# Kernel tuning notes

Hardware: AMD Instinct MI355X
Metric: run time of the kernel (lower is better)

The kernel has to match this reference:

```python
import jax, jax.numpy as jnp
import numpy as np

B, T = 4096, 256
COND, INTV, H = 128, 64, 256


def _glorot(key, shape):
    fan_in = shape[0]
    return jax.random.normal(key, shape, dtype=jnp.float32) / np.sqrt(fan_in)


def setup_inputs() -> dict:
    key = jax.random.key(0)
    ks = jax.random.split(key, 20)
    inp = {
        "cond": jax.random.normal(ks[0], (B, COND), dtype=jnp.float32),
        "interval_feat": jax.random.normal(ks[1], (B, INTV), dtype=jnp.float32),
        "times": jnp.cumsum(jax.random.uniform(ks[2], (B, T), dtype=jnp.float32), axis=1),
        "seq_lens": jax.random.randint(ks[3], (B,), 1, T + 1),
        # seq_feature MLP: INTV -> 2*INTV -> 2*INTV -> INTV
        "w1": _glorot(ks[4], (INTV, 2 * INTV)), "b1": jnp.zeros((2 * INTV,), jnp.float32),
        "w2": _glorot(ks[5], (2 * INTV, 2 * INTV)), "b2": jnp.zeros((2 * INTV,), jnp.float32),
        "w3": _glorot(ks[6], (2 * INTV, INTV)), "b3": jnp.zeros((INTV,), jnp.float32),
        # h0 projection: (COND+INTV) -> H
        "w_h0": _glorot(ks[7], (COND + INTV, H)), "b_h0": jnp.zeros((H,), jnp.float32),
        # GRUCell (input dim 1), gate order r,z,n
        "w_ih": _glorot(ks[8], (1, 3 * H)), "b_ih": jnp.zeros((3 * H,), jnp.float32),
        "w_hh": _glorot(ks[9], (H, 3 * H)), "b_hh": jnp.zeros((3 * H,), jnp.float32),
        # head: H -> 2 (delta, stop logit)
        "w_head": _glorot(ks[10], (H, 2)), "b_head": jnp.zeros((2,), jnp.float32),
    }
    return inp


def reference(cond, interval_feat, times, seq_lens,
              w1, b1, w2, b2, w3, b3, w_h0, b_h0,
              w_ih, w_hh, b_ih, b_hh, w_head, b_head):
    # seq_feature MLP
    s = jax.nn.relu(interval_feat @ w1 + b1)
    s = jax.nn.relu(s @ w2 + b2)
    seq_emb = s @ w3 + b3
    # initial hidden state
    h0 = jnp.tanh(jnp.concatenate([cond, seq_emb], axis=-1) @ w_h0 + b_h0)  # (B,H)
    # ground-truth deltas; step 0 input is 0, step i>=1 input is gt_delta[:, i-1]
    gt_delta = jnp.diff(times, axis=1, prepend=jnp.zeros((times.shape[0], 1), times.dtype))  # (B,T)
    xs = jnp.concatenate([jnp.zeros((1, times.shape[0]), times.dtype), gt_delta.T], axis=0)  # (T+1,B)

    def step(h, x):
        gi = x[:, None] * w_ih[0] + b_ih          # (B,3H)
        gh = h @ w_hh + b_hh                       # (B,3H)
        gi_r, gi_z, gi_n = jnp.split(gi, 3, axis=-1)
        gh_r, gh_z, gh_n = jnp.split(gh, 3, axis=-1)
        r = jax.nn.sigmoid(gi_r + gh_r)
        z = jax.nn.sigmoid(gi_z + gh_z)
        n = jnp.tanh(gi_n + r * gh_n)
        h_new = (1.0 - z) * n + z * h
        out = h_new @ w_head + b_head              # (B,2)
        return h_new, out

    _, outs = jax.lax.scan(step, h0, xs)           # outs: (T+1,B,2)
    pred_delta = outs[:, :, 0].T                   # (B,T+1)
    stop_logits = outs[:, :, 1].T                  # (B,T+1)
    return pred_delta, stop_logits
```

## Files before the change

kernel.cpp:

```cpp
#include <hip/hip_runtime.h>
#include <cstddef>

typedef _Float16 f16x8 __attribute__((ext_vector_type(8)));
typedef float    f32x4 __attribute__((ext_vector_type(4)));

#define Bc 4096
#define Tc 256
#define NSTEP 257
#define RB 16
#define HSTR 264
#define FSTR 260
#define HEAD_OFF 393216

__device__ inline float sigm(float x)  { return __builtin_amdgcn_rcpf(1.f + __expf(-x)); }
__device__ inline float tanh_(float x) { return 1.f - 2.f * __builtin_amdgcn_rcpf(1.f + __expf(2.f * x)); }

__global__ __launch_bounds__(256) void build_frags(
    const float* __restrict__ w_hh, const float* __restrict__ w_head,
    _Float16* __restrict__ ws)
{
    int flat = blockIdx.x * 256 + threadIdx.x;
    if (blockIdx.x < 96) {
        int f    = flat >> 6;
        int lane = flat & 63;
        int kt   = f & 7;
        int nc   = (f >> 3) % 3;
        int trio = f / 24;
        int c     = nc * 256 + trio * 16 + (lane & 15);
        int kbase = kt * 32 + (lane >> 4) * 8;
        _Float16* dst = ws + (size_t)f * 512 + (size_t)lane * 8;
        #pragma unroll
        for (int j = 0; j < 8; ++j)
            dst[j] = (_Float16)w_hh[(size_t)(kbase + j) * 768 + c];
    } else {
        int idx = flat - 96 * 256;
        int kt   = idx >> 6;
        int lane = idx & 63;
        int col   = lane & 15;
        int kbase = kt * 32 + (lane >> 4) * 8;
        _Float16* dst = ws + HEAD_OFF / 2 + (size_t)kt * 512 + (size_t)lane * 8;
        #pragma unroll
        for (int j = 0; j < 8; ++j)
            dst[j] = (col < 2) ? (_Float16)w_head[(size_t)(kbase + j) * 2 + col]
                               : (_Float16)0.f;
    }
}

__global__ __attribute__((amdgpu_waves_per_eu(2, 2))) __launch_bounds__(512)
void gru_mfma(
    const float* __restrict__ cond, const float* __restrict__ ivf,
    const float* __restrict__ times,
    const float* __restrict__ w1, const float* __restrict__ b1,
    const float* __restrict__ w2, const float* __restrict__ b2,
    const float* __restrict__ w3, const float* __restrict__ b3,
    const float* __restrict__ wh0, const float* __restrict__ bh0,
    const float* __restrict__ w_ih, const float* __restrict__ b_ih,
    const float* __restrict__ b_hh, const float* __restrict__ b_head,
    const _Float16* __restrict__ wfrag,
    float* __restrict__ out)
{
    __shared__ __align__(16) _Float16 hA[RB * HSTR];
    __shared__ __align__(16) _Float16 hB[RB * HSTR];
    __shared__ float  hF[RB * FSTR];
    __shared__ __align__(16) float xs4[4 * NSTEP * 4];
    __shared__ __align__(16) _Float16 headB[4096];
    __shared__ float  gateC[256 * 8];
    __shared__ float  outbuf[2][2][RB][16];
    __shared__ float  bh2[2];
    __shared__ float  mlp1[RB * 128];
    __shared__ float  mlp2[RB * 128];
    __shared__ float  embS[RB * 64];

    const int tid  = threadIdx.x;
    const int w    = tid >> 6;
    const int lane = tid & 63;
    const int l15  = lane & 15;
    const int q    = lane >> 4;
    const int row0 = blockIdx.x * RB;

    for (int o = tid; o < RB * 128; o += 512) {
        int r = o >> 7, c = o & 127;
        float a = b1[c];
        #pragma unroll 4
        for (int k = 0; k < 64; ++k)
            a = fmaf(ivf[(size_t)(row0 + r) * 64 + k], w1[k * 128 + c], a);
        mlp1[o] = fmaxf(a, 0.f);
    }
    __syncthreads();
    for (int o = tid; o < RB * 128; o += 512) {
        int r = o >> 7, c = o & 127;
        float a = b2[c];
        #pragma unroll 4
        for (int k = 0; k < 128; ++k)
            a = fmaf(mlp1[r * 128 + k], w2[k * 128 + c], a);
        mlp2[o] = fmaxf(a, 0.f);
    }
    __syncthreads();
    for (int o = tid; o < RB * 64; o += 512) {
        int r = o >> 6, c = o & 63;
        float a = b3[c];
        #pragma unroll 4
        for (int k = 0; k < 128; ++k)
            a = fmaf(mlp2[r * 128 + k], w3[k * 64 + c], a);
        embS[o] = a;
    }
    __syncthreads();
    for (int o = tid; o < RB * 256; o += 512) {
        int r = o >> 8, c = o & 255;
        float a = bh0[c];
        #pragma unroll 4
        for (int k = 0; k < 128; ++k)
            a = fmaf(cond[(size_t)(row0 + r) * 128 + k], wh0[k * 256 + c], a);
        #pragma unroll 4
        for (int k = 0; k < 64; ++k)
            a = fmaf(embS[r * 64 + k], wh0[(128 + k) * 256 + c], a);
        float h = tanh_(a);
        hF[r * FSTR + c] = h;
        hA[r * HSTR + c] = (_Float16)h;
    }

    for (int o = tid; o < 4 * NSTEP; o += 512) {
        int qg = o / NSTEP, ii = o - qg * NSTEP;
        #pragma unroll
        for (int jj = 0; jj < 4; ++jj) {
            int r = qg * 4 + jj;
            float x = 0.f;
            if (ii >= 1) {
                float a = times[(size_t)(row0 + r) * Tc + (ii - 1)];
                float b = (ii >= 2) ? times[(size_t)(row0 + r) * Tc + (ii - 2)] : 0.f;
                x = a - b;
            }
            xs4[o * 4 + jj] = x;
        }
    }
    {
        const float4* src = (const float4*)(wfrag + HEAD_OFF / 2);
        ((float4*)headB)[tid] = src[tid];
    }
    for (int uu = tid; uu < 256; uu += 512) {
        gateC[uu * 8 + 0] = w_ih[uu];
        gateC[uu * 8 + 1] = w_ih[256 + uu];
        gateC[uu * 8 + 2] = w_ih[512 + uu];
        gateC[uu * 8 + 3] = b_ih[uu] + b_hh[uu];
        gateC[uu * 8 + 4] = b_ih[256 + uu] + b_hh[256 + uu];
        gateC[uu * 8 + 5] = b_ih[512 + uu];
        gateC[uu * 8 + 6] = b_hh[512 + uu];
        gateC[uu * 8 + 7] = 0.f;
    }
    if (tid < 2) bh2[tid] = b_head[tid];

    const int u0 = w * 32 + l15;
    const int u1 = u0 + 16;

    f16x8 Bf[2][3][8];
    #pragma unroll
    for (int p = 0; p < 2; ++p)
        #pragma unroll
        for (int nc = 0; nc < 3; ++nc)
            #pragma unroll
            for (int kt = 0; kt < 8; ++kt)
                Bf[p][nc][kt] = *(const f16x8*)(wfrag
                    + (size_t)(((2 * w + p) * 3 + nc) * 8 + kt) * 512
                    + (size_t)lane * 8);

    __syncthreads();

    auto STEP = [&](const _Float16* hc, _Float16* hn, int i) {
        if (i >= 2 && ((i - 2) & 15) == 15) {
            const int obase = i - 17;
            const int par   = (obase >> 4) & 1;
            const int e     = tid & 15;
            const int row   = (tid >> 4) & 15;
            const int plane = tid >> 8;
            out[(size_t)plane * ((size_t)Bc * NSTEP)
                + (size_t)(row0 + row) * NSTEP + obase + e]
                = outbuf[par][plane][row][e] + bh2[plane];
        }

        const bool doGh = (i < NSTEP);
        const bool doHd = (i >= 1) && (w == 0);

        f32x4 aR[2], aZ[2], aN[2];
        #pragma unroll
        for (int p = 0; p < 2; ++p) {
            aR[p] = (f32x4){0.f, 0.f, 0.f, 0.f};
            aZ[p] = (f32x4){0.f, 0.f, 0.f, 0.f};
            aN[p] = (f32x4){0.f, 0.f, 0.f, 0.f};
        }
        f32x4 aH = (f32x4){0.f, 0.f, 0.f, 0.f};

        const _Float16* abase = hc + l15 * HSTR + q * 8;
        #pragma unroll
        for (int kt = 0; kt < 8; ++kt) {
            f16x8 Af = *(const f16x8*)(abase + kt * 32);
            if (doGh) {
                #pragma unroll
                for (int p = 0; p < 2; ++p) {
                    aR[p] = __builtin_amdgcn_mfma_f32_16x16x32_f16(Af, Bf[p][0][kt], aR[p], 0, 0, 0);
                    aZ[p] = __builtin_amdgcn_mfma_f32_16x16x32_f16(Af, Bf[p][1][kt], aZ[p], 0, 0, 0);
                    aN[p] = __builtin_amdgcn_mfma_f32_16x16x32_f16(Af, Bf[p][2][kt], aN[p], 0, 0, 0);
                }
            }
            if (doHd) {
                f16x8 Bh = *(const f16x8*)(headB + kt * 512 + lane * 8);
                aH = __builtin_amdgcn_mfma_f32_16x16x32_f16(Af, Bh, aH, 0, 0, 0);
            }
        }

        if (doHd && l15 < 2) {
            const int o = i - 1;
            #pragma unroll
            for (int j = 0; j < 4; ++j)
                outbuf[(o >> 4) & 1][l15][q * 4 + j][o & 15] = aH[j];
        }

        if (doGh) {
            const f32x4 xv = *(const f32x4*)(xs4 + (q * NSTEP + i) * 4);
            #pragma unroll
            for (int p = 0; p < 2; ++p) {
                const int u = p ? u1 : u0;
                const f32x4 g0 = *(const f32x4*)(gateC + u * 8);
                const f32x4 g1 = *(const f32x4*)(gateC + u * 8 + 4);
                #pragma unroll
                for (int j = 0; j < 4; ++j) {
                    const int m = q * 4 + j;
                    const float x  = xv[j];
                    const float ho = hF[m * FSTR + u];
                    const float rr = sigm(fmaf(x, g0[0], g0[3]) + aR[p][j]);
                    const float zz = sigm(fmaf(x, g0[1], g1[0]) + aZ[p][j]);
                    const float nn = tanh_(fmaf(x, g0[2], g1[1]) + rr * (aN[p][j] + g1[2]));
                    const float hn_ = nn + zz * (ho - nn);
                    hF[m * FSTR + u] = hn_;
                    hn[m * HSTR + u] = (_Float16)hn_;
                }
            }
        }
        __syncthreads();
    };

    for (int i = 0; i < NSTEP + 1; i += 2) {
        STEP(hA, hB, i);
        STEP(hB, hA, i + 1);
    }

    {
        const int e     = tid & 15;
        const int row   = (tid >> 4) & 15;
        const int plane = tid >> 8;
        if (e < 1) {
            out[(size_t)plane * ((size_t)Bc * NSTEP)
                + (size_t)(row0 + row) * NSTEP + 256 + e]
                = outbuf[0][plane][row][e] + bh2[plane];
        }
    }
}

extern "C" void kernel_launch(void* const* d_in, const int* in_sizes, int n_in,
                              void* d_out, int out_size, void* d_ws, size_t ws_size,
                              hipStream_t stream) {
    const float* cond   = (const float*)d_in[0];
    const float* ivf    = (const float*)d_in[1];
    const float* times  = (const float*)d_in[2];
    const float* w1     = (const float*)d_in[4];
    const float* b1     = (const float*)d_in[5];
    const float* w2     = (const float*)d_in[6];
    const float* b2     = (const float*)d_in[7];
    const float* w3     = (const float*)d_in[8];
    const float* b3     = (const float*)d_in[9];
    const float* wh0    = (const float*)d_in[10];
    const float* bh0    = (const float*)d_in[11];
    const float* w_ih   = (const float*)d_in[12];
    const float* b_ih   = (const float*)d_in[13];
    const float* w_hh   = (const float*)d_in[14];
    const float* b_hh   = (const float*)d_in[15];
    const float* w_head = (const float*)d_in[16];
    const float* b_head = (const float*)d_in[17];

    float*    outp = (float*)d_out;
    _Float16* ws   = (_Float16*)d_ws;

    build_frags<<<98, 256, 0, stream>>>(w_hh, w_head, ws);
    gru_mfma<<<Bc / RB, 512, 0, stream>>>(cond, ivf, times,
                                          w1, b1, w2, b2, w3, b3, wh0, bh0,
                                          w_ih, b_ih, b_hh, b_head,
                                          (const _Float16*)ws, outp);
}
```

Before: 769.2 us.

## Keep fp32 hidden state in registers and interleave gate columns for paired fp16 stores

The fp32 hidden state moves from shared memory into per-thread registers, and the weight fragments are rebuilt so each lane owns two adjacent hidden units, which allows packed f16x2 stores. The double-buffered fp16 hidden tile is replaced by a single buffer with an extra barrier per step between the MFMA reads and the gate writes. The aim is to remove shared-memory traffic for the fp32 state and halve the store count, at the cost of a second __syncthreads per timestep.

```diff
diff --git a/kernel.cpp b/kernel.cpp
--- a/kernel.cpp
+++ b/kernel.cpp
@@ -2,6 +2,7 @@
 #include <cstddef>
 
 typedef _Float16 f16x8 __attribute__((ext_vector_type(8)));
+typedef _Float16 f16x2 __attribute__((ext_vector_type(2)));
 typedef float    f32x4 __attribute__((ext_vector_type(4)));
 
 #define Bc 4096
@@ -9,7 +10,7 @@
 #define NSTEP 257
 #define RB 16
 #define HSTR 264
-#define FSTR 260
+#define GSTR 12
 #define HEAD_OFF 393216
 
 __device__ inline float sigm(float x)  { return __builtin_amdgcn_rcpf(1.f + __expf(-x)); }
@@ -26,7 +27,7 @@
         int kt   = f & 7;
         int nc   = (f >> 3) % 3;
         int trio = f / 24;
-        int c     = nc * 256 + trio * 16 + (lane & 15);
+        int c     = nc * 256 + (trio >> 1) * 32 + 2 * (lane & 15) + (trio & 1);
         int kbase = kt * 32 + (lane >> 4) * 8;
         _Float16* dst = ws + (size_t)f * 512 + (size_t)lane * 8;
         #pragma unroll
@@ -59,17 +60,16 @@
     const _Float16* __restrict__ wfrag,
     float* __restrict__ out)
 {
-    __shared__ __align__(16) _Float16 hA[RB * HSTR];
-    __shared__ __align__(16) _Float16 hB[RB * HSTR];
-    __shared__ float  hF[RB * FSTR];
+    __shared__ __align__(16) _Float16 h16[RB * HSTR];
     __shared__ __align__(16) float xs4[4 * NSTEP * 4];
     __shared__ __align__(16) _Float16 headB[4096];
-    __shared__ float  gateC[256 * 8];
+    __shared__ __align__(16) float gateC[256 * GSTR];
     __shared__ float  outbuf[2][2][RB][16];
     __shared__ float  bh2[2];
     __shared__ float  mlp1[RB * 128];
     __shared__ float  mlp2[RB * 128];
     __shared__ float  embS[RB * 64];
+    __shared__ float  h0f[RB * 256];
 
     const int tid  = threadIdx.x;
     const int w    = tid >> 6;
@@ -115,8 +115,8 @@
         for (int k = 0; k < 64; ++k)
             a = fmaf(embS[r * 64 + k], wh0[(128 + k) * 256 + c], a);
         float h = tanh_(a);
-        hF[r * FSTR + c] = h;
-        hA[r * HSTR + c] = (_Float16)h;
+        h0f[o] = h;
+        h16[r * HSTR + c] = (_Float16)h;
     }
 
     for (int o = tid; o < 4 * NSTEP; o += 512) {
@@ -138,19 +138,19 @@
         ((float4*)headB)[tid] = src[tid];
     }
     for (int uu = tid; uu < 256; uu += 512) {
-        gateC[uu * 8 + 0] = w_ih[uu];
-        gateC[uu * 8 + 1] = w_ih[256 + uu];
-        gateC[uu * 8 + 2] = w_ih[512 + uu];
-        gateC[uu * 8 + 3] = b_ih[uu] + b_hh[uu];
-        gateC[uu * 8 + 4] = b_ih[256 + uu] + b_hh[256 + uu];
-        gateC[uu * 8 + 5] = b_ih[512 + uu];
-        gateC[uu * 8 + 6] = b_hh[512 + uu];
-        gateC[uu * 8 + 7] = 0.f;
+        gateC[uu * GSTR + 0] = w_ih[uu];
+        gateC[uu * GSTR + 1] = w_ih[256 + uu];
+        gateC[uu * GSTR + 2] = w_ih[512 + uu];
+        gateC[uu * GSTR + 3] = b_ih[uu] + b_hh[uu];
+        gateC[uu * GSTR + 4] = b_ih[256 + uu] + b_hh[256 + uu];
+        gateC[uu * GSTR + 5] = b_ih[512 + uu];
+        gateC[uu * GSTR + 6] = b_hh[512 + uu];
+        gateC[uu * GSTR + 7] = 0.f;
     }
     if (tid < 2) bh2[tid] = b_head[tid];
 
-    const int u0 = w * 32 + l15;
-    const int u1 = u0 + 16;
+    const int u0 = w * 32 + 2 * l15;
+    const int u1 = u0 + 1;
 
     f16x8 Bf[2][3][8];
     #pragma unroll
@@ -165,8 +165,18 @@
 
     __syncthreads();
 
-    auto STEP = [&](const _Float16* hc, _Float16* hn, int i) {
-        if (i >= 2 && ((i - 2) & 15) == 15) {
+    float hold[2][4];
+    #pragma unroll
+    for (int p = 0; p < 2; ++p)
+        #pragma unroll
+        for (int j = 0; j < 4; ++j)
+            hold[p][j] = h0f[(q * 4 + j) * 256 + u0 + p];
+
+    for (int i = 0; i <= NSTEP; ++i) {
+        const bool doGh = (i < NSTEP);
+        const bool doHd = (i >= 1) && (w == 0);
+
+        if (i >= 17 && ((i - 17) & 15) == 0) {
             const int obase = i - 17;
             const int par   = (obase >> 4) & 1;
             const int e     = tid & 15;
@@ -177,9 +187,6 @@
                 = outbuf[par][plane][row][e] + bh2[plane];
         }
 
-        const bool doGh = (i < NSTEP);
-        const bool doHd = (i >= 1) && (w == 0);
-
         f32x4 aR[2], aZ[2], aN[2];
         #pragma unroll
         for (int p = 0; p < 2; ++p) {
@@ -189,21 +196,23 @@
         }
         f32x4 aH = (f32x4){0.f, 0.f, 0.f, 0.f};
 
-        const _Float16* abase = hc + l15 * HSTR + q * 8;
+        const _Float16* abase = h16 + l15 * HSTR + q * 8;
         #pragma unroll
         for (int kt = 0; kt < 8; ++kt) {
-            f16x8 Af = *(const f16x8*)(abase + kt * 32);
-            if (doGh) {
-                #pragma unroll
-                for (int p = 0; p < 2; ++p) {
-                    aR[p] = __builtin_amdgcn_mfma_f32_16x16x32_f16(Af, Bf[p][0][kt], aR[p], 0, 0, 0);
-                    aZ[p] = __builtin_amdgcn_mfma_f32_16x16x32_f16(Af, Bf[p][1][kt], aZ[p], 0, 0, 0);
-                    aN[p] = __builtin_amdgcn_mfma_f32_16x16x32_f16(Af, Bf[p][2][kt], aN[p], 0, 0, 0);
+            if (doGh || doHd) {
+                f16x8 Af = *(const f16x8*)(abase + kt * 32);
+                if (doGh) {
+                    #pragma unroll
+                    for (int p = 0; p < 2; ++p) {
+                        aR[p] = __builtin_amdgcn_mfma_f32_16x16x32_f16(Af, Bf[p][0][kt], aR[p], 0, 0, 0);
+                        aZ[p] = __builtin_amdgcn_mfma_f32_16x16x32_f16(Af, Bf[p][1][kt], aZ[p], 0, 0, 0);
+                        aN[p] = __builtin_amdgcn_mfma_f32_16x16x32_f16(Af, Bf[p][2][kt], aN[p], 0, 0, 0);
+                    }
                 }
-            }
-            if (doHd) {
-                f16x8 Bh = *(const f16x8*)(headB + kt * 512 + lane * 8);
-                aH = __builtin_amdgcn_mfma_f32_16x16x32_f16(Af, Bh, aH, 0, 0, 0);
+                if (doHd) {
+                    f16x8 Bh = *(const f16x8*)(headB + kt * 512 + lane * 8);
+                    aH = __builtin_amdgcn_mfma_f32_16x16x32_f16(Af, Bh, aH, 0, 0, 0);
+                }
             }
         }
 
@@ -214,33 +223,35 @@
                 outbuf[(o >> 4) & 1][l15][q * 4 + j][o & 15] = aH[j];
         }
 
+        __syncthreads();
+
         if (doGh) {
-            const f32x4 xv = *(const f32x4*)(xs4 + (q * NSTEP + i) * 4);
+            const f32x4 xv  = *(const f32x4*)(xs4 + (q * NSTEP + i) * 4);
+            const f32x4 g0a = *(const f32x4*)(gateC + u0 * GSTR);
+            const f32x4 g1a = *(const f32x4*)(gateC + u0 * GSTR + 4);
+            const f32x4 g0b = *(const f32x4*)(gateC + u1 * GSTR);
+            const f32x4 g1b = *(const f32x4*)(gateC + u1 * GSTR + 4);
             #pragma unroll
-            for (int p = 0; p < 2; ++p) {
-                const int u = p ? u1 : u0;
-                const f32x4 g0 = *(const f32x4*)(gateC + u * 8);
-                const f32x4 g1 = *(const f32x4*)(gateC + u * 8 + 4);
-                #pragma unroll
-                for (int j = 0; j < 4; ++j) {
-                    const int m = q * 4 + j;
-                    const float x  = xv[j];
-                    const float ho = hF[m * FSTR + u];
-                    const float rr = sigm(fmaf(x, g0[0], g0[3]) + aR[p][j]);
-                    const float zz = sigm(fmaf(x, g0[1], g1[0]) + aZ[p][j]);
-                    const float nn = tanh_(fmaf(x, g0[2], g1[1]) + rr * (aN[p][j] + g1[2]));
-                    const float hn_ = nn + zz * (ho - nn);
-                    hF[m * FSTR + u] = hn_;
-                    hn[m * HSTR + u] = (_Float16)hn_;
-                }
+            for (int j = 0; j < 4; ++j) {
+                const int m = q * 4 + j;
+                const float x = xv[j];
+
+                const float rr0 = sigm(fmaf(x, g0a[0], g0a[3]) + aR[0][j]);
+                const float zz0 = sigm(fmaf(x, g0a[1], g1a[0]) + aZ[0][j]);
+                const float nn0 = tanh_(fmaf(x, g0a[2], g1a[1]) + rr0 * (aN[0][j] + g1a[2]));
+                const float h0_ = nn0 + zz0 * (hold[0][j] - nn0);
+                hold[0][j] = h0_;
+
+                const float rr1 = sigm(fmaf(x, g0b[0], g0b[3]) + aR[1][j]);
+                const float zz1 = sigm(fmaf(x, g0b[1], g1b[0]) + aZ[1][j]);
+                const float nn1 = tanh_(fmaf(x, g0b[2], g1b[1]) + rr1 * (aN[1][j] + g1b[2]));
+                const float h1_ = nn1 + zz1 * (hold[1][j] - nn1);
+                hold[1][j] = h1_;
+
+                *(f16x2*)(h16 + m * HSTR + u0) = (f16x2){(_Float16)h0_, (_Float16)h1_};
             }
         }
         __syncthreads();
-    };
-
-    for (int i = 0; i < NSTEP + 1; i += 2) {
-        STEP(hA, hB, i);
-        STEP(hB, hA, i + 1);
     }
 
     {
```

Measured after the change: 705.1 us. 1.09x faster.
